# Performance work log

Measured on AMD Instinct MI355X. Metric: run time of the kernel, lower is better.

Reference implementation:

```python
import jax, jax.numpy as jnp
import numpy as np

EMBED_DIM = 1024
NUM_HEADS = 16
HEAD_DIM = EMBED_DIM // NUM_HEADS
B, S = 2, 2048


def setup_inputs() -> dict:
    key = jax.random.key(0)
    ks = jax.random.split(key, 9)
    s = 1.0 / np.sqrt(EMBED_DIM)
    return {
        "x": jax.random.normal(ks[0], (B, S, EMBED_DIM), dtype=jnp.float32),
        "Wq": jax.random.normal(ks[1], (EMBED_DIM, EMBED_DIM), dtype=jnp.float32) * s,
        "bq": jnp.zeros((EMBED_DIM,), dtype=jnp.float32),
        "Wk": jax.random.normal(ks[2], (EMBED_DIM, EMBED_DIM), dtype=jnp.float32) * s,
        "bk": jnp.zeros((EMBED_DIM,), dtype=jnp.float32),
        "Wv": jax.random.normal(ks[3], (EMBED_DIM, EMBED_DIM), dtype=jnp.float32) * s,
        "bv": jnp.zeros((EMBED_DIM,), dtype=jnp.float32),
        "Wo": jax.random.normal(ks[4], (EMBED_DIM, EMBED_DIM), dtype=jnp.float32) * s,
        "bo": jnp.zeros((EMBED_DIM,), dtype=jnp.float32),
    }


def reference(x, Wq, bq, Wk, bk, Wv, bv, Wo, bo):
    b, s, _ = x.shape
    # Projections; reshape to [B, H, S, Dh]
    def proj(W, bias):
        return (x @ W + bias).reshape(b, s, NUM_HEADS, HEAD_DIM).transpose(0, 2, 1, 3)
    q = proj(Wq, bq)
    k = proj(Wk, bk)
    v = proj(Wv, bv)
    scale = 1.0 / np.sqrt(HEAD_DIM).astype(np.float32)
    scores = jnp.einsum('bhqd,bhkd->bhqk', q, k) * scale  # [B,H,S,S]
    attn = jax.nn.softmax(scores, axis=-1)
    out = jnp.einsum('bhqk,bhkd->bhqd', attn, v)  # [B,H,S,Dh]
    out = out.transpose(0, 2, 1, 3).reshape(b, s, EMBED_DIM)
    return out @ Wo + bo
```

## Files before the change

kernel.cpp:

```cpp
#include <hip/hip_runtime.h>
#include <hip/hip_bf16.h>

typedef unsigned short ushort_t;
typedef __attribute__((ext_vector_type(4))) short short4v;
typedef __attribute__((ext_vector_type(8))) short short8;
typedef __attribute__((ext_vector_type(4))) float f32x4;
typedef __attribute__((ext_vector_type(16))) float f32x16;
typedef __attribute__((ext_vector_type(2))) unsigned int uint2v;

#define EMBED 1024
#define NHEAD 16
#define HDIM 64
#define BB 2
#define SSEQ 2048
#define MROWS (BB*SSEQ)
#define QKV_N (3*EMBED)
#define PER_BUF (MROWS*EMBED)

__device__ __forceinline__ ushort_t f2bf(float f) {
    union { float f; unsigned int u; } x; x.f = f;
    unsigned int r = x.u + 0x7fffu + ((x.u >> 16) & 1u);
    return (ushort_t)(r >> 16);
}
__device__ __forceinline__ unsigned cvt_pk_bf16(float lo, float hi) {
    unsigned r;
    asm("v_cvt_pk_bf16_f32 %0, %1, %2" : "=v"(r) : "v"(lo), "v"(hi));
    return r;
}

__device__ __forceinline__ void gload16(const void* g, void* l) {
    __builtin_amdgcn_global_load_lds(
        (const __attribute__((address_space(1))) unsigned int*)g,
        (__attribute__((address_space(3))) unsigned int*)l, 16, 0, 0);
}

__global__ void cast_bf16_kernel(const float* __restrict__ in, ushort_t* __restrict__ out, int n) {
    int i = (blockIdx.x * blockDim.x + threadIdx.x) * 4;
    if (i + 3 < n) {
        float4 v = *(const float4*)(in + i);
        out[i+0] = f2bf(v.x); out[i+1] = f2bf(v.y);
        out[i+2] = f2bf(v.z); out[i+3] = f2bf(v.w);
    }
}

__global__ void transpose_cast4_kernel(
    const float* __restrict__ W0, const float* __restrict__ W1,
    const float* __restrict__ W2, const float* __restrict__ W3,
    ushort_t* __restrict__ T0, ushort_t* __restrict__ T1,
    ushort_t* __restrict__ T2, ushort_t* __restrict__ T3)
{
    __shared__ float tile[32][33];
    int z = blockIdx.z;
    const float* W = (z == 0) ? W0 : (z == 1) ? W1 : (z == 2) ? W2 : W3;
    ushort_t* Wt   = (z == 0) ? T0 : (z == 1) ? T1 : (z == 2) ? T2 : T3;
    int tx = threadIdx.x, ty = threadIdx.y;
    int n0 = blockIdx.x * 32, k0 = blockIdx.y * 32;
    #pragma unroll
    for (int i = 0; i < 4; i++)
        tile[ty*4+i][tx] = W[(size_t)(k0 + ty*4 + i) * EMBED + n0 + tx];
    __syncthreads();
    #pragma unroll
    for (int i = 0; i < 4; i++)
        Wt[(size_t)(n0 + ty*4 + i) * EMBED + k0 + tx] = f2bf(tile[tx][ty*4+i]);
}

template<int OUT_MODE>
__global__ __launch_bounds__(256) void gemm_bt_kernel(
    const ushort_t* __restrict__ A,
    const ushort_t* __restrict__ Bt,
    const float* __restrict__ b0, const float* __restrict__ b1, const float* __restrict__ b2,
    void* __restrict__ Cout,
    ushort_t* __restrict__ vt_out,
    int M, int N, int K)
{
    __shared__ __attribute__((aligned(16))) ushort_t Asm[128*64];
    __shared__ __attribute__((aligned(16))) ushort_t Bsm[128*64];
    int t = threadIdx.x;
    int w = t >> 6, l = t & 63;
    int wr = w >> 1, wc = w & 1;
    int lrow = l & 15, lhi = l >> 4;

    int gx = gridDim.x;
    int flat = blockIdx.y * gx + blockIdx.x;
    int q8 = (gx * gridDim.y) >> 3;
    int nf = (flat & 7) * q8 + (flat >> 3);
    int m0 = (nf / gx) * 128, n0 = (nf % gx) * 128;

    int srow8 = l >> 3;
    int colel = 8 * ((l & 7) ^ srow8);

    f32x4 acc[4][4];
    #pragma unroll
    for (int mi = 0; mi < 4; mi++)
        #pragma unroll
        for (int ni = 0; ni < 4; ni++)
            #pragma unroll
            for (int c = 0; c < 4; c++) acc[mi][ni][c] = 0.f;

    for (int k0 = 0; k0 < K; k0 += 64) {
        __syncthreads();
        #pragma unroll
        for (int p = 0; p < 4; p++) {
            int row = w*32 + p*8 + srow8;
            gload16(&A [(size_t)(m0 + row)*K + k0 + colel], &Asm[(w*32 + p*8)*64]);
            gload16(&Bt[(size_t)(n0 + row)*K + k0 + colel], &Bsm[(w*32 + p*8)*64]);
        }
        __syncthreads();
        #pragma unroll
        for (int kk = 0; kk < 2; kk++) {
            short8 af[4], bfr[4];
            #pragma unroll
            for (int mi = 0; mi < 4; mi++) {
                int r = wr*64 + mi*16 + lrow;
                af[mi] = *(short8*)&Asm[r*64 + ((kk*32 + lhi*8) ^ ((r & 7) << 3))];
            }
            #pragma unroll
            for (int ni = 0; ni < 4; ni++) {
                int r = wc*64 + ni*16 + lrow;
                bfr[ni] = *(short8*)&Bsm[r*64 + ((kk*32 + lhi*8) ^ ((r & 7) << 3))];
            }
            __builtin_amdgcn_s_setprio(1);
            #pragma unroll
            for (int mi = 0; mi < 4; mi++)
                #pragma unroll
                for (int ni = 0; ni < 4; ni++)
                    acc[mi][ni] = __builtin_amdgcn_mfma_f32_16x16x32_bf16(af[mi], bfr[ni], acc[mi][ni], 0, 0, 0);
            __builtin_amdgcn_s_setprio(0);
        }
    }

    #pragma unroll
    for (int mi = 0; mi < 4; mi++)
        #pragma unroll
        for (int ni = 0; ni < 4; ni++) {
            int col = n0 + wc*64 + ni*16 + lrow;
            if (OUT_MODE == 2 && (col >> 10) == 2) {
                int hc = col & 1023;
                int h = hc >> 6, d = hc & 63;
                int row0 = m0 + wr*64 + mi*16 + lhi*4;
                int b = row0 >> 11, s0 = row0 & 2047;
                int bh = b*NHEAD + h;
                short4v pk;
                #pragma unroll
                for (int c = 0; c < 4; c++)
                    pk[c] = (short)f2bf(acc[mi][ni][c] + b2[hc]);
                *(short4v*)&vt_out[((size_t)bh*HDIM + d)*SSEQ + s0] = pk;
            } else {
                #pragma unroll
                for (int c = 0; c < 4; c++) {
                    int row = m0 + wr*64 + mi*16 + lhi*4 + c;
                    if (OUT_MODE == 0) {
                        float v = acc[mi][ni][c] + b0[col];
                        ((float*)Cout)[(size_t)row * N + col] = v;
                    } else {
                        int which = col >> 10, hc = col & 1023;
                        const float* bp = (which == 0) ? b0 : b1;
                        float v = acc[mi][ni][c] + bp[hc];
                        if (which == 0) v *= 0.18033688011112042f;
                        int h = hc >> 6, d = hc & 63;
                        int b = row >> 11, s = row & 2047;
                        ((ushort_t*)Cout)[(size_t)which*PER_BUF + ((size_t)((b*NHEAD + h)*SSEQ) + s)*HDIM + d] = f2bf(v);
                    }
                }
            }
        }
}

#define MFMA32(a,b,c) __builtin_amdgcn_mfma_f32_32x32x16_bf16(a, b, c, 0, 0, 0)

__global__ __launch_bounds__(512, 1) void flash_attn2_kernel(
    const ushort_t* __restrict__ q,
    const ushort_t* __restrict__ k,
    const ushort_t* __restrict__ vt,
    ushort_t* __restrict__ o)
{
    __shared__ __attribute__((aligned(16))) ushort_t Ks[2][2][64*64];
    __shared__ __attribute__((aligned(16))) ushort_t Vs[2][2][64*64];

    int t = threadIdx.x, w = t >> 6, l = t & 63;
    int l31 = l & 31, hi = l >> 5;

    int flat = blockIdx.x;
    int wg = (flat & 7) * 32 + (flat >> 3);
    int bh = wg >> 3;
    int q0 = (wg & 7) * 256;

    const ushort_t* qp = q  + (size_t)bh * SSEQ * HDIM;
    const ushort_t* kp = k  + (size_t)bh * SSEQ * HDIM;
    const ushort_t* vp = vt + (size_t)bh * HDIM * SSEQ;

    int lr = l >> 3, lc = l & 7;
    int colel = 8 * (lc ^ lr);

    short8 qf[4];
    int qrow = q0 + w*32 + l31;
    #pragma unroll
    for (int st = 0; st < 4; st++)
        qf[st] = *(const short8*)&qp[(size_t)qrow*HDIM + st*16 + hi*8];

    f32x16 o0 = {}, o1 = {};
    float m_run = -1e30f, l_run = 0.f;

    #define STAGE(buf, kv0) { \
        _Pragma("unroll") \
        for (int sub = 0; sub < 2; sub++) { \
            int row = w*8 + lr; \
            gload16(&kp[(size_t)(kv0 + sub*64 + row)*HDIM + colel], &Ks[buf][sub][(w*8)*64]); \
            gload16(&vp[(size_t)row*SSEQ + (kv0) + sub*64 + colel], &Vs[buf][sub][(w*8)*64]); \
        } }

    STAGE(0, 0)
    asm volatile("s_waitcnt vmcnt(0)");
    __syncthreads();
    int cur = 0;

    for (int kv0 = 0; kv0 < SSEQ; kv0 += 128) {
        if (kv0 + 128 < SSEQ) { STAGE(cur ^ 1, kv0 + 128) }

        f32x16 s0 = {}, s1 = {}, s2 = {}, s3 = {};
        __builtin_amdgcn_s_setprio(1);
        #pragma unroll
        for (int st = 0; st < 4; st++) {
            int colb = st*16 + hi*8;
            int sw0 = colb ^ ((l31 & 7) << 3);
            short8 kf0 = *(const short8*)&Ks[cur][0][l31*64        + sw0];
            short8 kf1 = *(const short8*)&Ks[cur][0][(32 + l31)*64 + sw0];
            short8 kf2 = *(const short8*)&Ks[cur][1][l31*64        + sw0];
            short8 kf3 = *(const short8*)&Ks[cur][1][(32 + l31)*64 + sw0];
            s0 = MFMA32(kf0, qf[st], s0);
            s1 = MFMA32(kf1, qf[st], s1);
            s2 = MFMA32(kf2, qf[st], s2);
            s3 = MFMA32(kf3, qf[st], s3);
        }
        __builtin_amdgcn_s_setprio(0);

        float ma = fmaxf(s0[0], s0[1]);
        float mb = fmaxf(s0[2], s0[3]);
        float mc = fmaxf(s0[4], s0[5]);
        float md = fmaxf(s0[6], s0[7]);
        ma = fmaxf(fmaxf(ma, s0[8]),  s0[9]);
        mb = fmaxf(fmaxf(mb, s0[10]), s0[11]);
        mc = fmaxf(fmaxf(mc, s0[12]), s0[13]);
        md = fmaxf(fmaxf(md, s0[14]), s0[15]);
        ma = fmaxf(fmaxf(ma, s1[0]),  s1[1]);
        mb = fmaxf(fmaxf(mb, s1[2]),  s1[3]);
        mc = fmaxf(fmaxf(mc, s1[4]),  s1[5]);
        md = fmaxf(fmaxf(md, s1[6]),  s1[7]);
        ma = fmaxf(fmaxf(ma, s1[8]),  s1[9]);
        mb = fmaxf(fmaxf(mb, s1[10]), s1[11]);
        mc = fmaxf(fmaxf(mc, s1[12]), s1[13]);
        md = fmaxf(fmaxf(md, s1[14]), s1[15]);
        ma = fmaxf(fmaxf(ma, s2[0]),  s2[1]);
        mb = fmaxf(fmaxf(mb, s2[2]),  s2[3]);
        mc = fmaxf(fmaxf(mc, s2[4]),  s2[5]);
        md = fmaxf(fmaxf(md, s2[6]),  s2[7]);
        ma = fmaxf(fmaxf(ma, s2[8]),  s2[9]);
        mb = fmaxf(fmaxf(mb, s2[10]), s2[11]);
        mc = fmaxf(fmaxf(mc, s2[12]), s2[13]);
        md = fmaxf(fmaxf(md, s2[14]), s2[15]);
        ma = fmaxf(fmaxf(ma, s3[0]),  s3[1]);
        mb = fmaxf(fmaxf(mb, s3[2]),  s3[3]);
        mc = fmaxf(fmaxf(mc, s3[4]),  s3[5]);
        md = fmaxf(fmaxf(md, s3[6]),  s3[7]);
        ma = fmaxf(fmaxf(ma, s3[8]),  s3[9]);
        mb = fmaxf(fmaxf(mb, s3[10]), s3[11]);
        mc = fmaxf(fmaxf(mc, s3[12]), s3[13]);
        md = fmaxf(fmaxf(md, s3[14]), s3[15]);
        float mx = fmaxf(fmaxf(ma, mb), fmaxf(mc, md));
        mx = fmaxf(mx, __shfl_xor(mx, 32));

        if (__any(mx > m_run + 8.f)) {
            float mnew = fmaxf(m_run, mx);
            float alpha = __builtin_amdgcn_exp2f(m_run - mnew);
            #pragma unroll
            for (int r = 0; r < 16; r++) { o0[r] *= alpha; o1[r] *= alpha; }
            l_run *= alpha;
            m_run = mnew;
        }
        float r0 = 0.f, r1 = 0.f, r2 = 0.f, r3 = 0.f;
        #pragma unroll
        for (int r = 0; r < 16; r += 4) {
            s0[r]   = __builtin_amdgcn_exp2f(s0[r]   - m_run); r0 += s0[r];
            s0[r+1] = __builtin_amdgcn_exp2f(s0[r+1] - m_run); r1 += s0[r+1];
            s0[r+2] = __builtin_amdgcn_exp2f(s0[r+2] - m_run); r2 += s0[r+2];
            s0[r+3] = __builtin_amdgcn_exp2f(s0[r+3] - m_run); r3 += s0[r+3];
        }
        #pragma unroll
        for (int r = 0; r < 16; r += 4) {
            s1[r]   = __builtin_amdgcn_exp2f(s1[r]   - m_run); r0 += s1[r];
            s1[r+1] = __builtin_amdgcn_exp2f(s1[r+1] - m_run); r1 += s1[r+1];
            s1[r+2] = __builtin_amdgcn_exp2f(s1[r+2] - m_run); r2 += s1[r+2];
            s1[r+3] = __builtin_amdgcn_exp2f(s1[r+3] - m_run); r3 += s1[r+3];
        }
        #pragma unroll
        for (int r = 0; r < 16; r += 4) {
            s2[r]   = __builtin_amdgcn_exp2f(s2[r]   - m_run); r0 += s2[r];
            s2[r+1] = __builtin_amdgcn_exp2f(s2[r+1] - m_run); r1 += s2[r+1];
            s2[r+2] = __builtin_amdgcn_exp2f(s2[r+2] - m_run); r2 += s2[r+2];
            s2[r+3] = __builtin_amdgcn_exp2f(s2[r+3] - m_run); r3 += s2[r+3];
        }
        #pragma unroll
        for (int r = 0; r < 16; r += 4) {
            s3[r]   = __builtin_amdgcn_exp2f(s3[r]   - m_run); r0 += s3[r];
            s3[r+1] = __builtin_amdgcn_exp2f(s3[r+1] - m_run); r1 += s3[r+1];
            s3[r+2] = __builtin_amdgcn_exp2f(s3[r+2] - m_run); r2 += s3[r+2];
            s3[r+3] = __builtin_amdgcn_exp2f(s3[r+3] - m_run); r3 += s3[r+3];
        }
        float rs = (r0 + r1) + (r2 + r3);
        rs += __shfl_xor(rs, 32);
        l_run += rs;

        short8 pfr[8];
        #define PACK8(SV, KS0) { \
            unsigned a0 = cvt_pk_bf16(SV[0], SV[1]); \
            unsigned a1 = cvt_pk_bf16(SV[2], SV[3]); \
            unsigned b0 = cvt_pk_bf16(SV[4], SV[5]); \
            unsigned b1 = cvt_pk_bf16(SV[6], SV[7]); \
            uint2v rr0 = __builtin_amdgcn_permlane32_swap(a0, b0, false, false); \
            uint2v rr1 = __builtin_amdgcn_permlane32_swap(a1, b1, false, false); \
            union { unsigned u[4]; short8 v; } pfa; \
            pfa.u[0] = rr0.x; pfa.u[1] = rr1.x; pfa.u[2] = rr0.y; pfa.u[3] = rr1.y; \
            pfr[KS0] = pfa.v; \
            unsigned c0 = cvt_pk_bf16(SV[8], SV[9]); \
            unsigned c1 = cvt_pk_bf16(SV[10], SV[11]); \
            unsigned d0 = cvt_pk_bf16(SV[12], SV[13]); \
            unsigned d1 = cvt_pk_bf16(SV[14], SV[15]); \
            uint2v rr2 = __builtin_amdgcn_permlane32_swap(c0, d0, false, false); \
            uint2v rr3 = __builtin_amdgcn_permlane32_swap(c1, d1, false, false); \
            union { unsigned u[4]; short8 v; } pfb; \
            pfb.u[0] = rr2.x; pfb.u[1] = rr3.x; pfb.u[2] = rr2.y; pfb.u[3] = rr3.y; \
            pfr[(KS0)+1] = pfb.v; \
        }
        PACK8(s0, 0)
        PACK8(s1, 2)
        PACK8(s2, 4)
        PACK8(s3, 6)
        #undef PACK8

        __builtin_amdgcn_s_setprio(1);
        #pragma unroll
        for (int ks = 0; ks < 8; ks++) {
            int sub = ks >> 2;
            int colb = (ks & 3)*16 + hi*8;
            int sw = colb ^ ((l31 & 7) << 3);
            short8 vf0 = *(const short8*)&Vs[cur][sub][l31*64        + sw];
            short8 vf1 = *(const short8*)&Vs[cur][sub][(32 + l31)*64 + sw];
            o0 = MFMA32(vf0, pfr[ks], o0);
            o1 = MFMA32(vf1, pfr[ks], o1);
        }
        __builtin_amdgcn_s_setprio(0);

        asm volatile("s_waitcnt vmcnt(0)");
        __syncthreads();
        cur ^= 1;
    }

    float rl = 1.f / l_run;
    ushort_t* Ot = ((ushort_t*)Ks) + w*(32*64);
    #pragma unroll
    for (int dt = 0; dt < 2; dt++)
        #pragma unroll
        for (int rq = 0; rq < 4; rq++) {
            float v0 = (dt ? o1[rq*4+0] : o0[rq*4+0]) * rl;
            float v1 = (dt ? o1[rq*4+1] : o0[rq*4+1]) * rl;
            float v2 = (dt ? o1[rq*4+2] : o0[rq*4+2]) * rl;
            float v3 = (dt ? o1[rq*4+3] : o0[rq*4+3]) * rl;
            int d0 = dt*32 + rq*8 + hi*4;
            uint2v pw = { cvt_pk_bf16(v0, v1), cvt_pk_bf16(v2, v3) };
            *(uint2v*)&Ot[l31*64 + (d0 ^ ((l31 & 7) << 3))] = pw;
        }

    int b = bh >> 4, h = bh & 15;
    int q2 = l >> 1, dh = (l & 1) * 32;
    size_t obase = ((size_t)(b*SSEQ) + q0 + w*32 + q2)*EMBED + h*HDIM;
    #pragma unroll
    for (int j = 0; j < 4; j++) {
        int d = dh + j*8;
        short8 ov = *(short8*)&Ot[q2*64 + (d ^ ((q2 & 7) << 3))];
        *(short8*)&o[obase + d] = ov;
    }
}

extern "C" void kernel_launch(void* const* d_in, const int* in_sizes, int n_in,
                              void* d_out, int out_size, void* d_ws, size_t ws_size,
                              hipStream_t stream) {
    const float* x  = (const float*)d_in[0];
    const float* Wq = (const float*)d_in[1];
    const float* bq = (const float*)d_in[2];
    const float* Wk = (const float*)d_in[3];
    const float* bk = (const float*)d_in[4];
    const float* Wv = (const float*)d_in[5];
    const float* bv = (const float*)d_in[6];
    const float* Wo = (const float*)d_in[7];
    const float* bo = (const float*)d_in[8];

    char* ws = (char*)d_ws;
    ushort_t* xb  = (ushort_t*)(ws);
    ushort_t* WqT = (ushort_t*)(ws + (8u  << 20));
    ushort_t* WkT = (ushort_t*)(ws + (10u << 20));
    ushort_t* WvT = (ushort_t*)(ws + (12u << 20));
    ushort_t* WoT = (ushort_t*)(ws + (14u << 20));
    ushort_t* qb  = (ushort_t*)(ws + (16u << 20));
    ushort_t* kb  = (ushort_t*)(ws + (24u << 20));
    ushort_t* vtb = (ushort_t*)(ws + (40u << 20));
    ushort_t* ab  = xb;

    int nx = MROWS * EMBED;
    cast_bf16_kernel<<<nx/(256*4), 256, 0, stream>>>(x, xb, nx);

    transpose_cast4_kernel<<<dim3(EMBED/32, EMBED/32, 4), dim3(32, 8), 0, stream>>>(
        Wq, Wk, Wv, Wo, WqT, WkT, WvT, WoT);

    gemm_bt_kernel<2><<<dim3(QKV_N/128, MROWS/128), 256, 0, stream>>>(
        xb, WqT, bq, bk, bv, qb, vtb, MROWS, QKV_N, EMBED);

    flash_attn2_kernel<<<256, 512, 0, stream>>>(qb, kb, vtb, ab);

    gemm_bt_kernel<0><<<dim3(EMBED/128, MROWS/128), 256, 0, stream>>>(
        ab, WoT, bo, bo, bo, d_out, nullptr, MROWS, EMBED, EMBED);
}
```

Measured before the change: 121.2 us.

## Use 256x256 double-buffered tile kernel for QKV projection GEMM

Replaces the templated 128x128 GEMM used for the QKV projection with a dedicated 256x256-tile kernel that runs 8 waves (512 threads), double-buffers LDS via async global-to-LDS loads, and fuses the Q/K and transposed-V epilogues. The output projection keeps the old 128x128 kernel, with the template mode logic stripped. The aim is higher arithmetic intensity per block and overlap of loads with MFMA. The trade-off is a grid of only 192 blocks at one block per CU, which may leave the 256 CUs underused.

New measurement: 127.3 us. 5.0% more time.

```diff
diff --git a/kernel.cpp b/kernel.cpp
--- a/kernel.cpp
+++ b/kernel.cpp
@@ -64,13 +64,135 @@
         Wt[(size_t)(n0 + ty*4 + i) * EMBED + k0 + tx] = f2bf(tile[tx][ty*4+i]);
 }
 
-template<int OUT_MODE>
-__global__ __launch_bounds__(256) void gemm_bt_kernel(
+__global__ __launch_bounds__(512, 1) void gemm_qkv_256_kernel(
     const ushort_t* __restrict__ A,
     const ushort_t* __restrict__ Bt,
     const float* __restrict__ b0, const float* __restrict__ b1, const float* __restrict__ b2,
-    void* __restrict__ Cout,
-    ushort_t* __restrict__ vt_out,
+    ushort_t* __restrict__ qk_out,
+    ushort_t* __restrict__ vt_out)
+{
+    __shared__ __attribute__((aligned(16))) ushort_t Am[2][256*64];
+    __shared__ __attribute__((aligned(16))) ushort_t Bm[2][256*64];
+    const int K = 1024, NT = 16;
+
+    int t = threadIdx.x, w = t >> 6, l = t & 63;
+    int wr = w >> 2, wc = w & 3;
+    int lrow = l & 15, lhi = l >> 4;
+    int lr = l >> 3;
+    int colel = 8 * ((l & 7) ^ lr);
+
+    int gx = gridDim.x;
+    int flat = blockIdx.y * gx + blockIdx.x;
+    int q8 = (gx * gridDim.y) >> 3;
+    int nf = (flat & 7) * q8 + (flat >> 3);
+    int m0 = (nf / gx) * 256, n0 = (nf % gx) * 256;
+
+    f32x4 acc[8][4];
+    #pragma unroll
+    for (int mi = 0; mi < 8; mi++)
+        #pragma unroll
+        for (int ni = 0; ni < 4; ni++)
+            #pragma unroll
+            for (int c = 0; c < 4; c++) acc[mi][ni][c] = 0.f;
+
+    #define STAGE256(buf, k0v) { \
+        _Pragma("unroll") \
+        for (int p = 0; p < 4; p++) { \
+            int row = w*32 + p*8 + lr; \
+            gload16(&A [(size_t)(m0 + row)*K + (k0v) + colel], &Am[buf][(w*32 + p*8)*64]); \
+            gload16(&Bt[(size_t)(n0 + row)*K + (k0v) + colel], &Bm[buf][(w*32 + p*8)*64]); \
+        } }
+
+    STAGE256(0, 0)
+    STAGE256(1, 64)
+    asm volatile("s_waitcnt vmcnt(8)" ::: "memory");
+    __builtin_amdgcn_sched_barrier(0);
+    asm volatile("s_barrier" ::: "memory");
+
+    for (int kt = 0; kt < NT; kt++) {
+        int cur = kt & 1;
+        const ushort_t* As = Am[cur];
+        const ushort_t* Bs = Bm[cur];
+
+        short8 bf[4][2];
+        #pragma unroll
+        for (int ni = 0; ni < 4; ni++)
+            #pragma unroll
+            for (int kk = 0; kk < 2; kk++) {
+                int r = wc*64 + ni*16 + lrow;
+                bf[ni][kk] = *(const short8*)&Bs[r*64 + ((kk*32 + lhi*8) ^ ((r & 7) << 3))];
+            }
+
+        #pragma unroll
+        for (int qd = 0; qd < 4; qd++) {
+            short8 af[2][2];
+            #pragma unroll
+            for (int m2 = 0; m2 < 2; m2++)
+                #pragma unroll
+                for (int kk = 0; kk < 2; kk++) {
+                    int r = wr*128 + (qd*2 + m2)*16 + lrow;
+                    af[m2][kk] = *(const short8*)&As[r*64 + ((kk*32 + lhi*8) ^ ((r & 7) << 3))];
+                }
+            __builtin_amdgcn_s_setprio(1);
+            #pragma unroll
+            for (int m2 = 0; m2 < 2; m2++)
+                #pragma unroll
+                for (int ni = 0; ni < 4; ni++)
+                    #pragma unroll
+                    for (int kk = 0; kk < 2; kk++)
+                        acc[qd*2 + m2][ni] = __builtin_amdgcn_mfma_f32_16x16x32_bf16(
+                            af[m2][kk], bf[ni][kk], acc[qd*2 + m2][ni], 0, 0, 0);
+            __builtin_amdgcn_s_setprio(0);
+        }
+
+        __builtin_amdgcn_sched_barrier(0);
+        asm volatile("s_barrier" ::: "memory");
+        if (kt + 2 < NT) {
+            STAGE256(cur, (kt + 2) * 64)
+            asm volatile("s_waitcnt vmcnt(8)" ::: "memory");
+        } else if (kt + 1 < NT) {
+            asm volatile("s_waitcnt vmcnt(0)" ::: "memory");
+        }
+        __builtin_amdgcn_sched_barrier(0);
+        asm volatile("s_barrier" ::: "memory");
+    }
+    #undef STAGE256
+
+    #pragma unroll
+    for (int mi = 0; mi < 8; mi++)
+        #pragma unroll
+        for (int ni = 0; ni < 4; ni++) {
+            int col = n0 + wc*64 + ni*16 + lrow;
+            int which = col >> 10, hc = col & 1023;
+            int h = hc >> 6, d = hc & 63;
+            if (which == 2) {
+                int row0 = m0 + wr*128 + mi*16 + lhi*4;
+                int b = row0 >> 11, s0 = row0 & 2047;
+                int bh = b*NHEAD + h;
+                short4v pk;
+                #pragma unroll
+                for (int c = 0; c < 4; c++)
+                    pk[c] = (short)f2bf(acc[mi][ni][c] + b2[hc]);
+                *(short4v*)&vt_out[((size_t)bh*HDIM + d)*SSEQ + s0] = pk;
+            } else {
+                const float* bp = (which == 0) ? b0 : b1;
+                #pragma unroll
+                for (int c = 0; c < 4; c++) {
+                    int row = m0 + wr*128 + mi*16 + lhi*4 + c;
+                    float v = acc[mi][ni][c] + bp[hc];
+                    if (which == 0) v *= 0.18033688011112042f;
+                    int b = row >> 11, s = row & 2047;
+                    qk_out[(size_t)which*PER_BUF + ((size_t)((b*NHEAD + h)*SSEQ) + s)*HDIM + d] = f2bf(v);
+                }
+            }
+        }
+}
+
+__global__ __launch_bounds__(256) void gemm_out_kernel(
+    const ushort_t* __restrict__ A,
+    const ushort_t* __restrict__ Bt,
+    const float* __restrict__ b0,
+    float* __restrict__ Cout,
     int M, int N, int K)
 {
     __shared__ __attribute__((aligned(16))) ushort_t Asm[128*64];
@@ -134,34 +256,10 @@
         #pragma unroll
         for (int ni = 0; ni < 4; ni++) {
             int col = n0 + wc*64 + ni*16 + lrow;
-            if (OUT_MODE == 2 && (col >> 10) == 2) {
-                int hc = col & 1023;
-                int h = hc >> 6, d = hc & 63;
-                int row0 = m0 + wr*64 + mi*16 + lhi*4;
-                int b = row0 >> 11, s0 = row0 & 2047;
-                int bh = b*NHEAD + h;
-                short4v pk;
-                #pragma unroll
-                for (int c = 0; c < 4; c++)
-                    pk[c] = (short)f2bf(acc[mi][ni][c] + b2[hc]);
-                *(short4v*)&vt_out[((size_t)bh*HDIM + d)*SSEQ + s0] = pk;
-            } else {
-                #pragma unroll
-                for (int c = 0; c < 4; c++) {
-                    int row = m0 + wr*64 + mi*16 + lhi*4 + c;
-                    if (OUT_MODE == 0) {
-                        float v = acc[mi][ni][c] + b0[col];
-                        ((float*)Cout)[(size_t)row * N + col] = v;
-                    } else {
-                        int which = col >> 10, hc = col & 1023;
-                        const float* bp = (which == 0) ? b0 : b1;
-                        float v = acc[mi][ni][c] + bp[hc];
-                        if (which == 0) v *= 0.18033688011112042f;
-                        int h = hc >> 6, d = hc & 63;
-                        int b = row >> 11, s = row & 2047;
-                        ((ushort_t*)Cout)[(size_t)which*PER_BUF + ((size_t)((b*NHEAD + h)*SSEQ) + s)*HDIM + d] = f2bf(v);
-                    }
-                }
+            #pragma unroll
+            for (int c = 0; c < 4; c++) {
+                int row = m0 + wr*64 + mi*16 + lhi*4 + c;
+                Cout[(size_t)row * N + col] = acc[mi][ni][c] + b0[col];
             }
         }
 }
@@ -404,6 +502,7 @@
     ushort_t* kb  = (ushort_t*)(ws + (24u << 20));
     ushort_t* vtb = (ushort_t*)(ws + (40u << 20));
     ushort_t* ab  = xb;
+    (void)kb;
 
     int nx = MROWS * EMBED;
     cast_bf16_kernel<<<nx/(256*4), 256, 0, stream>>>(x, xb, nx);
@@ -411,11 +510,11 @@
     transpose_cast4_kernel<<<dim3(EMBED/32, EMBED/32, 4), dim3(32, 8), 0, stream>>>(
         Wq, Wk, Wv, Wo, WqT, WkT, WvT, WoT);
 
-    gemm_bt_kernel<2><<<dim3(QKV_N/128, MROWS/128), 256, 0, stream>>>(
-        xb, WqT, bq, bk, bv, qb, vtb, MROWS, QKV_N, EMBED);
+    gemm_qkv_256_kernel<<<dim3(QKV_N/256, MROWS/256), 512, 0, stream>>>(
+        xb, WqT, bq, bk, bv, qb, vtb);
 
     flash_attn2_kernel<<<256, 512, 0, stream>>>(qb, kb, vtb, ab);
 
-    gemm_bt_kernel<0><<<dim3(EMBED/128, MROWS/128), 256, 0, stream>>>(
-        ab, WoT, bo, bo, bo, d_out, nullptr, MROWS, EMBED, EMBED);
-}
+    gemm_out_kernel<<<dim3(EMBED/128, MROWS/128), 256, 0, stream>>>(
+        ab, WoT, bo, (float*)d_out, MROWS, EMBED, EMBED);
+}
```
